# Performance work log

Measured on AMD Instinct MI355X. Metric: run time of the kernel, lower is better.

The kernel has to match this reference:

```python
import jax, jax.numpy as jnp
import numpy as np

B, T, C = 8, 1024, 576
NH, NKV = 9, 3          # query heads, kv heads
HD = C // NH            # 64 head dim
KVC = C // NKV          # 192 kv proj width
N_REP = NH // NKV       # 3


def setup_inputs() -> dict:
    key = jax.random.key(0)
    ks = jax.random.split(key, 9)
    s = 0.02
    return {
        "x": jax.random.normal(ks[0], (B, T, C), jnp.float32),
        "Wq": jax.random.normal(ks[1], (C, C), jnp.float32) * s,
        "bq": jax.random.normal(ks[2], (C,), jnp.float32) * s,
        "Wk": jax.random.normal(ks[3], (C, KVC), jnp.float32) * s,
        "bk": jax.random.normal(ks[4], (KVC,), jnp.float32) * s,
        "Wv": jax.random.normal(ks[5], (C, KVC), jnp.float32) * s,
        "bv": jax.random.normal(ks[6], (KVC,), jnp.float32) * s,
        "Wo": jax.random.normal(ks[7], (C, C), jnp.float32) * s,
        "bo": jax.random.normal(ks[8], (C,), jnp.float32) * s,
    }


def reference(x, Wq, bq, Wk, bk, Wv, bv, Wo, bo):
    Bx, Tx, Cx = x.shape
    q = x @ Wq + bq                                # [B,T,C]
    k = x @ Wk + bk                                # [B,T,KVC]
    v = x @ Wv + bv
    # split heads: q -> [B,NH,T,HD]; k,v -> [B,NKV,T,HD]
    q = q.reshape(Bx, Tx, NH, HD).transpose(0, 2, 1, 3)
    k = k.reshape(Bx, Tx, NKV, HD).transpose(0, 2, 1, 3)
    v = v.reshape(Bx, Tx, NKV, HD).transpose(0, 2, 1, 3)
    # repeat_kv: [B,NKV,T,HD] -> [B,NKV*N_REP,T,HD]
    k = jnp.repeat(k, N_REP, axis=1)
    v = jnp.repeat(v, N_REP, axis=1)
    att = jnp.einsum("bhqd,bhkd->bhqk", q, k) * (1.0 / np.sqrt(HD))
    mask = jnp.tril(jnp.ones((Tx, Tx), bool))
    att = jnp.where(mask, att, -jnp.inf)
    att = jax.nn.softmax(att, axis=-1)
    y = jnp.einsum("bhqk,bhkd->bhqd", att, v)      # [B,NH,T,HD]
    y = y.transpose(0, 2, 1, 3).reshape(Bx, Tx, Cx)
    return y @ Wo + bo
```

## Files before the change

kernel.cpp:

```cpp
#include <hip/hip_runtime.h>
#include <hip/hip_bf16.h>
#include <math.h>

#define B_    8
#define T_    1024
#define C_    576
#define NH_   9
#define NKV_  3
#define HD_   64
#define KVC_  192
#define NREP_ 3
#define NQKV_ 960
#define NTK_  9

typedef __attribute__((ext_vector_type(8))) short bf16x8;
typedef __attribute__((ext_vector_type(4))) float f32x4;
typedef __attribute__((ext_vector_type(4))) int i32x4;

#define MFMA_16x16x32(a, b, c) __builtin_amdgcn_mfma_f32_16x16x32_bf16((a), (b), (c), 0, 0, 0)

__device__ __forceinline__ ushort f2bf(float f) {
  __hip_bfloat16 h = __float2bfloat16(f);
  return *reinterpret_cast<const ushort*>(&h);
}

__device__ __forceinline__ float fexp2(float x) { return __builtin_amdgcn_exp2f(x); }

__device__ __forceinline__ int swz(int row, int col) {
  int byte = (row << 7) + (col << 1);
  return (byte ^ ((row & 7) << 4)) >> 1;
}

__device__ __forceinline__ void gload16(const ushort* g, ushort* l) {
  __builtin_amdgcn_global_load_lds(
      (const __attribute__((address_space(1))) unsigned int*)g,
      (__attribute__((address_space(3))) unsigned int*)l, 16, 0, 0);
}

__device__ __forceinline__ i32x4 packrow(const float* src) {
  const float4 a = *reinterpret_cast<const float4*>(src);
  const float4 b = *reinterpret_cast<const float4*>(src + 4);
  union { ushort u[8]; i32x4 v; } t;
  t.u[0] = f2bf(a.x); t.u[1] = f2bf(a.y); t.u[2] = f2bf(a.z); t.u[3] = f2bf(a.w);
  t.u[4] = f2bf(b.x); t.u[5] = f2bf(b.y); t.u[6] = f2bf(b.z); t.u[7] = f2bf(b.w);
  return t.v;
}

__global__ __launch_bounds__(256) void convert_x_kernel(
    const float* __restrict__ x, ushort* __restrict__ xbt) {
  const int tm = blockIdx.x, tk = blockIdx.y;
  ushort* dst = xbt + ((size_t)tm * NTK_ + tk) * 8192;
  #pragma unroll
  for (int i = 0; i < 4; i++) {
    const int c = threadIdx.x + i * 256;
    const int row = c >> 3, colb = (c & 7) * 8;
    *reinterpret_cast<i32x4*>(&dst[swz(row, colb)]) =
        packrow(x + (size_t)(tm * 128 + row) * C_ + tk * 64 + colb);
  }
}

__global__ __launch_bounds__(256) void convert_w_kernel(
    const float* __restrict__ Wq, const float* __restrict__ Wk,
    const float* __restrict__ Wv, const float* __restrict__ Wo,
    const float* __restrict__ bq, const float* __restrict__ bk,
    const float* __restrict__ bv, const float* __restrict__ bo,
    ushort* __restrict__ wqkvT, ushort* __restrict__ woT, float* __restrict__ bcat) {
  const int tnc = blockIdx.x, tk = blockIdx.y;
  #pragma unroll
  for (int i = 0; i < 2; i++) {
    const int c = threadIdx.x + i * 256;
    const int row = c >> 3, colb = (c & 7) * 8;
    const float* src; int ld; ushort* dst; int ncol;
    if (tnc < 15) {
      const int n = tnc * 64 + row;
      if (n < 576)      { src = Wq; ld = C_;  ncol = n; }
      else if (n < 768) { src = Wk; ld = KVC_; ncol = n - 576; }
      else              { src = Wv; ld = KVC_; ncol = n - 768; }
      dst = wqkvT + ((size_t)tnc * NTK_ + tk) * 4096;
    } else {
      src = Wo; ld = C_; ncol = (tnc - 15) * 64 + row;
      dst = woT + ((size_t)(tnc - 15) * NTK_ + tk) * 4096;
    }
    union { ushort u[8]; i32x4 v; } t;
    #pragma unroll
    for (int e = 0; e < 8; e++)
      t.u[e] = f2bf(src[(size_t)(tk * 64 + colb + e) * ld + ncol]);
    *reinterpret_cast<i32x4*>(&dst[swz(row, colb)]) = t.v;
    if (tk == 0 && (c & 7) == 0) {
      const int n = tnc * 64 + row;
      float bv_;
      if (n < 576)       bv_ = bq[n];
      else if (n < 768)  bv_ = bk[n - 576];
      else if (n < 960)  bv_ = bv[n - 768];
      else               bv_ = bo[n - 960];
      bcat[n] = bv_;
    }
  }
}

template<bool OUT_BF16>
__global__ __launch_bounds__(256) void gemm_lds_kernel(
    const ushort* __restrict__ At, const ushort* __restrict__ Bt,
    const float* __restrict__ bias, void* __restrict__ Cp,
    int N, int q_cols) {
  const int nwg = gridDim.x * gridDim.y;
  const int flat = blockIdx.y * gridDim.x + blockIdx.x;
  const int wg = (flat & 7) * (nwg >> 3) + (flat >> 3);
  const int bxs = wg % gridDim.x, bys = wg / gridDim.x;

  __shared__ ushort As[128 * 64];
  __shared__ ushort Bs[64 * 64];
  const int bm = bys * 128, bn = bxs * 64;
  const int tid = threadIdx.x;
  const int wave = tid >> 6, lane = tid & 63;
  const int lg = lane >> 4, ll = lane & 15;
  const int wm = (wave >> 1) * 64, wn = (wave & 1) * 32;
  f32x4 acc[4][2] = {};

  const ushort* abase = At + (size_t)bys * NTK_ * 8192;
  const ushort* bbase = Bt + (size_t)bxs * NTK_ * 4096;

  for (int kt = 0; kt < NTK_; kt++) {
    const ushort* ak = abase + (size_t)kt * 8192;
    const ushort* bk = bbase + (size_t)kt * 4096;
    #pragma unroll
    for (int i = 0; i < 4; i++) {
      const int c0 = (wave << 6) + (i << 8);
      gload16(ak + (size_t)(c0 + lane) * 8, &As[c0 * 8]);
    }
    #pragma unroll
    for (int i = 0; i < 2; i++) {
      const int c0 = (wave << 6) + (i << 8);
      gload16(bk + (size_t)(c0 + lane) * 8, &Bs[c0 * 8]);
    }
    __syncthreads();

    bf16x8 af[4][2], bfr[2][2];
    #pragma unroll
    for (int mt = 0; mt < 4; mt++) {
      af[mt][0] = *reinterpret_cast<const bf16x8*>(&As[swz(wm + mt * 16 + ll, lg * 8)]);
      af[mt][1] = *reinterpret_cast<const bf16x8*>(&As[swz(wm + mt * 16 + ll, 32 + lg * 8)]);
    }
    #pragma unroll
    for (int nt = 0; nt < 2; nt++) {
      bfr[nt][0] = *reinterpret_cast<const bf16x8*>(&Bs[swz(wn + nt * 16 + ll, lg * 8)]);
      bfr[nt][1] = *reinterpret_cast<const bf16x8*>(&Bs[swz(wn + nt * 16 + ll, 32 + lg * 8)]);
    }
    #pragma unroll
    for (int mt = 0; mt < 4; mt++) {
      #pragma unroll
      for (int nt = 0; nt < 2; nt++) {
        acc[mt][nt] = MFMA_16x16x32(af[mt][0], bfr[nt][0], acc[mt][nt]);
        acc[mt][nt] = MFMA_16x16x32(af[mt][1], bfr[nt][1], acc[mt][nt]);
      }
    }
    __syncthreads();
  }

  #pragma unroll
  for (int mt = 0; mt < 4; mt++) {
    #pragma unroll
    for (int nt = 0; nt < 2; nt++) {
      const int col = bn + wn + nt * 16 + ll;
      const float scale = (col < q_cols) ? 0.18033688011112042f : 1.0f;
      #pragma unroll
      for (int r = 0; r < 4; r++) {
        const int row = bm + wm + mt * 16 + lg * 4 + r;
        const float val = (acc[mt][nt][r] + bias[col]) * scale;
        if (OUT_BF16) ((ushort*)Cp)[(size_t)row * N + col] = f2bf(val);
        else          ((float*)Cp)[(size_t)row * N + col] = val;
      }
    }
  }
}

__global__ __launch_bounds__(256) void attn_mfma_kernel(
    const ushort* __restrict__ qkv, ushort* __restrict__ yt) {
  const int qt = 15 - blockIdx.z, h = blockIdx.x, b = blockIdx.y;
  const int kvh = h / NREP_;
  const int tid = threadIdx.x;
  const int wave = tid >> 6, lane = tid & 63;
  const int lg = lane >> 4, ll = lane & 15;
  const int w16 = wave << 4;
  const int qrow0 = qt << 6;
  const int nk = (qt + 2) >> 1;

  __shared__ ushort Ks[2][64 * 64];
  __shared__ ushort Vts[2][64 * 64];
  __shared__ ushort Ps[4][16 * 64];

  const int ksub = tid >> 7, ktt = tid & 127;
  const int kr = ktt >> 2, kcb = (ktt & 3) << 4;
  const int vkp = ktt & 31, vds = (ktt >> 5) << 4;

  const ushort* qrow = qkv + (size_t)(b * T_ + qrow0 + w16 + ll) * NQKV_ + h * HD_;
  const bf16x8 qa0 = *reinterpret_cast<const bf16x8*>(qrow + lg * 8);
  const bf16x8 qa1 = *reinterpret_cast<const bf16x8*>(qrow + 32 + lg * 8);

  f32x4 o[4] = {};
  float m_i = -INFINITY, l_i = 0.f;

  i32x4 kra, krb, krc, krd, va0, va1, vb0, vb1;
  {
    const size_t rb = (size_t)(b * T_);
    const ushort* ks0 = qkv + (rb + ksub * 64 + kr) * NQKV_ + 576 + kvh * HD_ + kcb;
    const ushort* ks1 = ks0 + (size_t)32 * NQKV_;
    kra = *reinterpret_cast<const i32x4*>(ks0);
    krb = *reinterpret_cast<const i32x4*>(ks0 + 8);
    krc = *reinterpret_cast<const i32x4*>(ks1);
    krd = *reinterpret_cast<const i32x4*>(ks1 + 8);
    const ushort* v0 = qkv + (rb + ksub * 64 + vkp * 2) * NQKV_ + 768 + kvh * HD_ + vds;
    const ushort* v1 = v0 + NQKV_;
    va0 = *reinterpret_cast<const i32x4*>(v0); va1 = *reinterpret_cast<const i32x4*>(v0 + 8);
    vb0 = *reinterpret_cast<const i32x4*>(v1); vb1 = *reinterpret_cast<const i32x4*>(v1 + 8);
  }
  {
    *reinterpret_cast<i32x4*>(&Ks[ksub][swz(kr, kcb)]) = kra;
    *reinterpret_cast<i32x4*>(&Ks[ksub][swz(kr, kcb + 8)]) = krb;
    *reinterpret_cast<i32x4*>(&Ks[ksub][swz(kr + 32, kcb)]) = krc;
    *reinterpret_cast<i32x4*>(&Ks[ksub][swz(kr + 32, kcb + 8)]) = krd;
    union { i32x4 v; ushort u[8]; } a0, a1, c0, c1;
    a0.v = va0; a1.v = va1; c0.v = vb0; c1.v = vb1;
    #pragma unroll
    for (int e = 0; e < 8; e++) {
      *reinterpret_cast<uint*>(&Vts[ksub][swz(vds + e, vkp * 2)]) =
          (uint)a0.u[e] | ((uint)c0.u[e] << 16);
      *reinterpret_cast<uint*>(&Vts[ksub][swz(vds + 8 + e, vkp * 2)]) =
          (uint)a1.u[e] | ((uint)c1.u[e] << 16);
    }
  }
  __syncthreads();

  #pragma unroll 1
  for (int kt = 0; kt < nk; kt++) {
    if (kt + 1 < nk) {
      const size_t rb = (size_t)(b * T_ + ((kt + 1) << 7));
      const ushort* ks0 = qkv + (rb + ksub * 64 + kr) * NQKV_ + 576 + kvh * HD_ + kcb;
      const ushort* ks1 = ks0 + (size_t)32 * NQKV_;
      kra = *reinterpret_cast<const i32x4*>(ks0);
      krb = *reinterpret_cast<const i32x4*>(ks0 + 8);
      krc = *reinterpret_cast<const i32x4*>(ks1);
      krd = *reinterpret_cast<const i32x4*>(ks1 + 8);
      const ushort* v0 = qkv + (rb + ksub * 64 + vkp * 2) * NQKV_ + 768 + kvh * HD_ + vds;
      const ushort* v1 = v0 + NQKV_;
      va0 = *reinterpret_cast<const i32x4*>(v0); va1 = *reinterpret_cast<const i32x4*>(v0 + 8);
      vb0 = *reinterpret_cast<const i32x4*>(v1); vb1 = *reinterpret_cast<const i32x4*>(v1 + 8);
    }

    f32x4 s[8];
    #pragma unroll
    for (int kc = 0; kc < 8; kc++) {
      const int sub = kc >> 2, kcl = kc & 3;
      const bf16x8 kb0 = *reinterpret_cast<const bf16x8*>(&Ks[sub][swz(kcl * 16 + ll, lg * 8)]);
      const bf16x8 kb1 = *reinterpret_cast<const bf16x8*>(&Ks[sub][swz(kcl * 16 + ll, 32 + lg * 8)]);
      f32x4 z = {};
      z = MFMA_16x16x32(kb0, qa0, z);
      s[kc] = MFMA_16x16x32(kb1, qa1, z);
    }

    if (kt == nk - 1) {
      const int qg = qrow0 + w16 + ll - (kt << 7);
      #pragma unroll
      for (int kc = 0; kc < 8; kc++)
        #pragma unroll
        for (int r = 0; r < 4; r++)
          if (kc * 16 + lg * 4 + r > qg) s[kc][r] = -INFINITY;
    }

    float mA[8];
    #pragma unroll
    for (int kc = 0; kc < 8; kc++)
      mA[kc] = fmaxf(fmaxf(s[kc][0], s[kc][1]), fmaxf(s[kc][2], s[kc][3]));
    float t0 = fmaxf(fmaxf(fmaxf(mA[0], mA[1]), fmaxf(mA[2], mA[3])),
                     fmaxf(fmaxf(mA[4], mA[5]), fmaxf(mA[6], mA[7])));
    t0 = fmaxf(t0, __shfl_xor(t0, 16));
    t0 = fmaxf(t0, __shfl_xor(t0, 32));
    if (!__all(t0 <= m_i + 11.5415603f)) {
      const float mn = fmaxf(m_i, t0);
      const float al = fexp2(m_i - mn);
      m_i = mn;
      l_i *= al;
      #pragma unroll
      for (int r = 0; r < 4; r++) {
        const float ar = __shfl(al, lg * 4 + r);
        o[0][r] *= ar; o[1][r] *= ar; o[2][r] *= ar; o[3][r] *= ar;
      }
    }

    float rsub[2];
    ushort* Pw = Ps[wave];
    #pragma unroll
    for (int sub = 0; sub < 2; sub++) {
      float rk[4];
      #pragma unroll
      for (int kcl = 0; kcl < 4; kcl++) {
        const int kc = sub * 4 + kcl;
        float p0 = fexp2(s[kc][0] - m_i);
        float p1 = fexp2(s[kc][1] - m_i);
        float p2 = fexp2(s[kc][2] - m_i);
        float p3 = fexp2(s[kc][3] - m_i);
        rk[kcl] = (p0 + p1) + (p2 + p3);
        uint w01 = (uint)f2bf(p0) | ((uint)f2bf(p1) << 16);
        uint w23 = (uint)f2bf(p2) | ((uint)f2bf(p3) << 16);
        *reinterpret_cast<uint*>(&Pw[swz(ll, kcl * 16 + lg * 4)])     = w01;
        *reinterpret_cast<uint*>(&Pw[swz(ll, kcl * 16 + lg * 4 + 2)]) = w23;
      }
      rsub[sub] = (rk[0] + rk[1]) + (rk[2] + rk[3]);
      #pragma unroll
      for (int khl = 0; khl < 2; khl++) {
        const bf16x8 pa = *reinterpret_cast<const bf16x8*>(&Pw[swz(ll, khl * 32 + lg * 8)]);
        #pragma unroll
        for (int d0 = 0; d0 < 4; d0++) {
          const bf16x8 vbr = *reinterpret_cast<const bf16x8*>(&Vts[sub][swz(d0 * 16 + ll, khl * 32 + lg * 8)]);
          o[d0] = MFMA_16x16x32(pa, vbr, o[d0]);
        }
      }
    }
    float rs = rsub[0] + rsub[1];
    rs += __shfl_xor(rs, 16);
    rs += __shfl_xor(rs, 32);
    l_i += rs;

    if (kt + 1 < nk) {
      __syncthreads();
      *reinterpret_cast<i32x4*>(&Ks[ksub][swz(kr, kcb)]) = kra;
      *reinterpret_cast<i32x4*>(&Ks[ksub][swz(kr, kcb + 8)]) = krb;
      *reinterpret_cast<i32x4*>(&Ks[ksub][swz(kr + 32, kcb)]) = krc;
      *reinterpret_cast<i32x4*>(&Ks[ksub][swz(kr + 32, kcb + 8)]) = krd;
      union { i32x4 v; ushort u[8]; } a0, a1, c0, c1;
      a0.v = va0; a1.v = va1; c0.v = vb0; c1.v = vb1;
      #pragma unroll
      for (int e = 0; e < 8; e++) {
        *reinterpret_cast<uint*>(&Vts[ksub][swz(vds + e, vkp * 2)]) =
            (uint)a0.u[e] | ((uint)c0.u[e] << 16);
        *reinterpret_cast<uint*>(&Vts[ksub][swz(vds + 8 + e, vkp * 2)]) =
            (uint)a1.u[e] | ((uint)c1.u[e] << 16);
      }
      __syncthreads();
    }
  }

  #pragma unroll
  for (int r = 0; r < 4; r++) {
    const float lr = __shfl(l_i, lg * 4 + r);
    const float inv = 1.f / lr;
    const int rowg = b * T_ + qrow0 + w16 + lg * 4 + r;
    ushort* ybase = yt + ((size_t)(rowg >> 7) * NTK_ + h) * 8192;
    const int lrow = rowg & 127;
    #pragma unroll
    for (int d0 = 0; d0 < 4; d0++) {
      ybase[swz(lrow, d0 * 16 + ll)] = f2bf(o[d0][r] * inv);
    }
  }
}

extern "C" void kernel_launch(void* const* d_in, const int* in_sizes, int n_in,
                              void* d_out, int out_size, void* d_ws, size_t ws_size,
                              hipStream_t stream) {
  const float* x  = (const float*)d_in[0];
  const float* Wq = (const float*)d_in[1];
  const float* bq = (const float*)d_in[2];
  const float* Wk = (const float*)d_in[3];
  const float* bk = (const float*)d_in[4];
  const float* Wv = (const float*)d_in[5];
  const float* bv = (const float*)d_in[6];
  const float* Wo = (const float*)d_in[7];
  const float* bo = (const float*)d_in[8];
  float* out = (float*)d_out;

  const int M = B_ * T_;
  ushort* wqkvT = (ushort*)d_ws;
  ushort* woT   = wqkvT + (size_t)15 * NTK_ * 4096;
  float*  bcat  = (float*)(woT + (size_t)9 * NTK_ * 4096);
  ushort* qkv   = (ushort*)(bcat + 1536);
  ushort* yt    = qkv + (size_t)M * NQKV_;
  ushort* xbt   = yt + (size_t)M * C_;

  convert_w_kernel<<<dim3(24, NTK_), 256, 0, stream>>>(Wq, Wk, Wv, Wo, bq, bk, bv, bo,
                                                       wqkvT, woT, bcat);
  convert_x_kernel<<<dim3(M / 128, NTK_), 256, 0, stream>>>(x, xbt);
  gemm_lds_kernel<true><<<dim3(NQKV_ / 64, M / 128), 256, 0, stream>>>(
      xbt, wqkvT, bcat, qkv, NQKV_, 576);
  attn_mfma_kernel<<<dim3(NH_, B_, 16), 256, 0, stream>>>(qkv, yt);
  gemm_lds_kernel<false><<<dim3(C_ / 64, M / 128), 256, 0, stream>>>(
      yt, woT, bcat + NQKV_, out, C_, 0);
}
```

Baseline: 76.54 us.

## Write K and pre-transposed V in swizzled tile layout from QKV GEMM epilogue

The QKV projection epilogue now writes Q to its own buffer and scatters K and V into per-(batch, kv-head, 64-row) tiles already in the swizzled LDS layout, with V stored transposed. The attention kernel then copies those tiles straight into LDS with direct global-to-LDS loads instead of doing register staging, transposition and repacking. This removes the per-iteration transpose and shuffle work from attention. The cost is scattered 2-byte stores in the GEMM epilogue and the loss of the register prefetch double-buffering, so the loads are now issued synchronously each iteration.

New measurement: 72.32 us. 1.06x faster.

```diff
diff --git a/kernel.cpp b/kernel.cpp
--- a/kernel.cpp
+++ b/kernel.cpp
@@ -98,11 +98,11 @@
   }
 }
 
-template<bool OUT_BF16>
+template<int MODE>
 __global__ __launch_bounds__(256) void gemm_lds_kernel(
     const ushort* __restrict__ At, const ushort* __restrict__ Bt,
     const float* __restrict__ bias, void* __restrict__ Cp,
-    int N, int q_cols) {
+    ushort* __restrict__ ktv, ushort* __restrict__ vtv, int N) {
   const int nwg = gridDim.x * gridDim.y;
   const int flat = blockIdx.y * gridDim.x + blockIdx.x;
   const int wg = (flat & 7) * (nwg >> 3) + (flat >> 3);
@@ -162,20 +162,33 @@
     #pragma unroll
     for (int nt = 0; nt < 2; nt++) {
       const int col = bn + wn + nt * 16 + ll;
-      const float scale = (col < q_cols) ? 0.18033688011112042f : 1.0f;
       #pragma unroll
       for (int r = 0; r < 4; r++) {
         const int row = bm + wm + mt * 16 + lg * 4 + r;
-        const float val = (acc[mt][nt][r] + bias[col]) * scale;
-        if (OUT_BF16) ((ushort*)Cp)[(size_t)row * N + col] = f2bf(val);
-        else          ((float*)Cp)[(size_t)row * N + col] = val;
+        const float val = acc[mt][nt][r] + bias[col];
+        if (MODE == 0) {
+          ((float*)Cp)[(size_t)row * N + col] = val;
+        } else {
+          if (col < 576) {
+            ((ushort*)Cp)[(size_t)row * C_ + col] = f2bf(val * 0.18033688011112042f);
+          } else if (col < 768) {
+            const int kvh = (col - 576) >> 6, d = (col - 576) & 63;
+            ushort* t = ktv + (((size_t)(row >> 10) * 3 + kvh) * 16 + ((row >> 6) & 15)) * 4096;
+            t[swz(row & 63, d)] = f2bf(val);
+          } else {
+            const int kvh = (col - 768) >> 6, d = (col - 768) & 63;
+            ushort* t = vtv + (((size_t)(row >> 10) * 3 + kvh) * 16 + ((row >> 6) & 15)) * 4096;
+            t[swz(d, row & 63)] = f2bf(val);
+          }
+        }
       }
     }
   }
 }
 
 __global__ __launch_bounds__(256) void attn_mfma_kernel(
-    const ushort* __restrict__ qkv, ushort* __restrict__ yt) {
+    const ushort* __restrict__ qb, const ushort* __restrict__ ktv,
+    const ushort* __restrict__ vtv, ushort* __restrict__ yt) {
   const int qt = 15 - blockIdx.z, h = blockIdx.x, b = blockIdx.y;
   const int kvh = h / NREP_;
   const int tid = threadIdx.x;
@@ -185,67 +198,34 @@
   const int qrow0 = qt << 6;
   const int nk = (qt + 2) >> 1;
 
-  __shared__ ushort Ks[2][64 * 64];
-  __shared__ ushort Vts[2][64 * 64];
-  __shared__ ushort Ps[4][16 * 64];
-
-  const int ksub = tid >> 7, ktt = tid & 127;
-  const int kr = ktt >> 2, kcb = (ktt & 3) << 4;
-  const int vkp = ktt & 31, vds = (ktt >> 5) << 4;
-
-  const ushort* qrow = qkv + (size_t)(b * T_ + qrow0 + w16 + ll) * NQKV_ + h * HD_;
+  __shared__ ushort Ks[2][4096];
+  __shared__ ushort Vts[2][4096];
+  __shared__ ushort Ps[4][1024];
+
+  const ushort* ktb = ktv + ((size_t)b * 3 + kvh) * 16 * 4096;
+  const ushort* vtb = vtv + ((size_t)b * 3 + kvh) * 16 * 4096;
+
+  const ushort* qrow = qb + (size_t)(b * T_ + qrow0 + w16 + ll) * C_ + h * HD_;
   const bf16x8 qa0 = *reinterpret_cast<const bf16x8*>(qrow + lg * 8);
   const bf16x8 qa1 = *reinterpret_cast<const bf16x8*>(qrow + 32 + lg * 8);
 
   f32x4 o[4] = {};
   float m_i = -INFINITY, l_i = 0.f;
 
-  i32x4 kra, krb, krc, krd, va0, va1, vb0, vb1;
-  {
-    const size_t rb = (size_t)(b * T_);
-    const ushort* ks0 = qkv + (rb + ksub * 64 + kr) * NQKV_ + 576 + kvh * HD_ + kcb;
-    const ushort* ks1 = ks0 + (size_t)32 * NQKV_;
-    kra = *reinterpret_cast<const i32x4*>(ks0);
-    krb = *reinterpret_cast<const i32x4*>(ks0 + 8);
-    krc = *reinterpret_cast<const i32x4*>(ks1);
-    krd = *reinterpret_cast<const i32x4*>(ks1 + 8);
-    const ushort* v0 = qkv + (rb + ksub * 64 + vkp * 2) * NQKV_ + 768 + kvh * HD_ + vds;
-    const ushort* v1 = v0 + NQKV_;
-    va0 = *reinterpret_cast<const i32x4*>(v0); va1 = *reinterpret_cast<const i32x4*>(v0 + 8);
-    vb0 = *reinterpret_cast<const i32x4*>(v1); vb1 = *reinterpret_cast<const i32x4*>(v1 + 8);
-  }
-  {
-    *reinterpret_cast<i32x4*>(&Ks[ksub][swz(kr, kcb)]) = kra;
-    *reinterpret_cast<i32x4*>(&Ks[ksub][swz(kr, kcb + 8)]) = krb;
-    *reinterpret_cast<i32x4*>(&Ks[ksub][swz(kr + 32, kcb)]) = krc;
-    *reinterpret_cast<i32x4*>(&Ks[ksub][swz(kr + 32, kcb + 8)]) = krd;
-    union { i32x4 v; ushort u[8]; } a0, a1, c0, c1;
-    a0.v = va0; a1.v = va1; c0.v = vb0; c1.v = vb1;
-    #pragma unroll
-    for (int e = 0; e < 8; e++) {
-      *reinterpret_cast<uint*>(&Vts[ksub][swz(vds + e, vkp * 2)]) =
-          (uint)a0.u[e] | ((uint)c0.u[e] << 16);
-      *reinterpret_cast<uint*>(&Vts[ksub][swz(vds + 8 + e, vkp * 2)]) =
-          (uint)a1.u[e] | ((uint)c1.u[e] << 16);
-    }
-  }
-  __syncthreads();
-
   #pragma unroll 1
   for (int kt = 0; kt < nk; kt++) {
-    if (kt + 1 < nk) {
-      const size_t rb = (size_t)(b * T_ + ((kt + 1) << 7));
-      const ushort* ks0 = qkv + (rb + ksub * 64 + kr) * NQKV_ + 576 + kvh * HD_ + kcb;
-      const ushort* ks1 = ks0 + (size_t)32 * NQKV_;
-      kra = *reinterpret_cast<const i32x4*>(ks0);
-      krb = *reinterpret_cast<const i32x4*>(ks0 + 8);
-      krc = *reinterpret_cast<const i32x4*>(ks1);
-      krd = *reinterpret_cast<const i32x4*>(ks1 + 8);
-      const ushort* v0 = qkv + (rb + ksub * 64 + vkp * 2) * NQKV_ + 768 + kvh * HD_ + vds;
-      const ushort* v1 = v0 + NQKV_;
-      va0 = *reinterpret_cast<const i32x4*>(v0); va1 = *reinterpret_cast<const i32x4*>(v0 + 8);
-      vb0 = *reinterpret_cast<const i32x4*>(v1); vb1 = *reinterpret_cast<const i32x4*>(v1 + 8);
-    }
+    #pragma unroll
+    for (int sub = 0; sub < 2; sub++) {
+      const ushort* ks = ktb + (size_t)(2 * kt + sub) * 4096;
+      const ushort* vs = vtb + (size_t)(2 * kt + sub) * 4096;
+      #pragma unroll
+      for (int i = 0; i < 2; i++) {
+        const int c0 = (wave << 6) + (i << 8);
+        gload16(ks + (size_t)(c0 + lane) * 8, &Ks[sub][c0 * 8]);
+        gload16(vs + (size_t)(c0 + lane) * 8, &Vts[sub][c0 * 8]);
+      }
+    }
+    __syncthreads();
 
     f32x4 s[8];
     #pragma unroll
@@ -321,23 +301,7 @@
     rs += __shfl_xor(rs, 32);
     l_i += rs;
 
-    if (kt + 1 < nk) {
-      __syncthreads();
-      *reinterpret_cast<i32x4*>(&Ks[ksub][swz(kr, kcb)]) = kra;
-      *reinterpret_cast<i32x4*>(&Ks[ksub][swz(kr, kcb + 8)]) = krb;
-      *reinterpret_cast<i32x4*>(&Ks[ksub][swz(kr + 32, kcb)]) = krc;
-      *reinterpret_cast<i32x4*>(&Ks[ksub][swz(kr + 32, kcb + 8)]) = krd;
-      union { i32x4 v; ushort u[8]; } a0, a1, c0, c1;
-      a0.v = va0; a1.v = va1; c0.v = vb0; c1.v = vb1;
-      #pragma unroll
-      for (int e = 0; e < 8; e++) {
-        *reinterpret_cast<uint*>(&Vts[ksub][swz(vds + e, vkp * 2)]) =
-            (uint)a0.u[e] | ((uint)c0.u[e] << 16);
-        *reinterpret_cast<uint*>(&Vts[ksub][swz(vds + 8 + e, vkp * 2)]) =
-            (uint)a1.u[e] | ((uint)c1.u[e] << 16);
-      }
-      __syncthreads();
-    }
+    __syncthreads();
   }
 
   #pragma unroll
@@ -372,16 +336,18 @@
   ushort* wqkvT = (ushort*)d_ws;
   ushort* woT   = wqkvT + (size_t)15 * NTK_ * 4096;
   float*  bcat  = (float*)(woT + (size_t)9 * NTK_ * 4096);
-  ushort* qkv   = (ushort*)(bcat + 1536);
-  ushort* yt    = qkv + (size_t)M * NQKV_;
+  ushort* qb    = (ushort*)(bcat + 1536);
+  ushort* ktv   = qb + (size_t)M * C_;
+  ushort* vtv   = ktv + (size_t)B_ * NKV_ * 16 * 4096;
+  ushort* yt    = vtv + (size_t)B_ * NKV_ * 16 * 4096;
   ushort* xbt   = yt + (size_t)M * C_;
 
   convert_w_kernel<<<dim3(24, NTK_), 256, 0, stream>>>(Wq, Wk, Wv, Wo, bq, bk, bv, bo,
                                                        wqkvT, woT, bcat);
   convert_x_kernel<<<dim3(M / 128, NTK_), 256, 0, stream>>>(x, xbt);
-  gemm_lds_kernel<true><<<dim3(NQKV_ / 64, M / 128), 256, 0, stream>>>(
-      xbt, wqkvT, bcat, qkv, NQKV_, 576);
-  attn_mfma_kernel<<<dim3(NH_, B_, 16), 256, 0, stream>>>(qkv, yt);
-  gemm_lds_kernel<false><<<dim3(C_ / 64, M / 128), 256, 0, stream>>>(
-      yt, woT, bcat + NQKV_, out, C_, 0);
-}
+  gemm_lds_kernel<1><<<dim3(NQKV_ / 64, M / 128), 256, 0, stream>>>(
+      xbt, wqkvT, bcat, qb, ktv, vtv, NQKV_);
+  attn_mfma_kernel<<<dim3(NH_, B_, 16), 256, 0, stream>>>(qb, ktv, vtv, yt);
+  gemm_lds_kernel<0><<<dim3(C_ / 64, M / 128), 256, 0, stream>>>(
+      yt, woT, bcat + NQKV_, out, nullptr, nullptr, C_);
+}
```
